# Kernel optimization log

Hardware: AMD Instinct MI355X
Metric: run time of the kernel (lower is better)

The kernel has to match this reference:

```python
import jax, jax.numpy as jnp
import numpy as np
from math import ceil, sqrt

# Inner module: Linear(2048,4096)+ReLU, Linear(4096,4096)+ReLU, Linear(4096,2048)
D_IN, D_H, D_OUT = 2048, 4096, 2048
BATCH = 4096
# named_modules() order: each Linear yields weight then bias; ReLU skipped
SHAPES = [(D_H, D_IN), (D_H,), (D_H, D_H), (D_H,), (D_OUT, D_H), (D_OUT,)]
NUM_P = sum(int(np.prod(s)) for s in SHAPES)  # 33_566_720
SIZE_N = ceil(sqrt(NUM_P))                    # 5794
SIZE_M = ceil(1.0 * SIZE_N / 2)               # 2897 (compress = 1.0)


def setup_inputs() -> dict:
    key = jax.random.key(0)
    k1, k2, k3 = jax.random.split(key, 3)
    k = sqrt(12) / 2 * SIZE_M ** (-0.25)  # norm_V init bound
    V1 = jax.random.uniform(k1, (SIZE_N, SIZE_M), jnp.float32, -k, k)
    V2 = jax.random.uniform(k2, (SIZE_M, SIZE_N), jnp.float32, -k, k)
    x = jax.random.normal(k3, (BATCH, D_IN), jnp.float32)
    return {"x": x, "V1": V1, "V2": V2}


def _unpack(Vf):
    # scatter-copy: contiguous slices of flattened V -> weights/biases in traversal order
    params, i = [], 0
    for s in SHAPES:
        n = int(np.prod(s))
        params.append(Vf[i:i + n].reshape(s))
        i += n
    return params


def reference(x, V1, V2):
    # WandBtoV: low-rank reconstruction then per-element copy into weights (fused here)
    Vf = (V1 @ V2).reshape(-1)  # [SIZE_N*SIZE_N]; only first NUM_P elements used
    W1, b1, W2, b2, W3, b3 = _unpack(Vf)
    h = jax.nn.relu(x @ W1.T + b1)   # [B, D_H]
    h = jax.nn.relu(h @ W2.T + b2)   # [B, D_H]
    return h @ W3.T + b3             # [B, D_OUT]
```

## Files before the change

### kernel.cpp

```cpp
#include <hip/hip_runtime.h>
#include <stdint.h>

typedef __attribute__((ext_vector_type(8)))  __bf16 bf16x8;
typedef __attribute__((ext_vector_type(16))) float  f32x16;
typedef unsigned short u16;
typedef __attribute__((ext_vector_type(8))) unsigned short u16x8;

#define GLOBAL_AS __attribute__((address_space(1)))
#define LDS_AS    __attribute__((address_space(3)))

__device__ __forceinline__ void load_lds16(const void* g, void* l) {
    __builtin_amdgcn_global_load_lds((const GLOBAL_AS void*)g, (LDS_AS void*)l, 16, 0, 0);
}

__device__ __forceinline__ u16 f2bf(float f) {
    union { float f; uint32_t u; } v; v.f = f;
    uint32_t r = v.u + 0x7FFFu + ((v.u >> 16) & 1u);
    return (u16)(r >> 16);
}
__device__ __forceinline__ float b2f(u16 b) {
    union { uint32_t u; float f; } v; v.u = ((uint32_t)b) << 16;
    return v.f;
}

__global__ void k_conv_pad(const float* __restrict__ in, u16* __restrict__ out,
                           int rIn, int cIn, int cOut, int total8) {
    int idx = blockIdx.x * blockDim.x + threadIdx.x;
    if (idx >= total8) return;
    int c8n = cOut >> 3;
    int r  = idx / c8n;
    int c0 = (idx - r * c8n) << 3;
    u16x8 o;
#pragma unroll
    for (int j = 0; j < 8; ++j) {
        int c = c0 + j;
        o[j] = (r < rIn && c < cIn) ? f2bf(in[(size_t)r * cIn + c]) : (u16)0;
    }
    *(u16x8*)(out + (size_t)r * cOut + c0) = o;
}

__global__ void k_transpose_conv(const float* __restrict__ in, u16* __restrict__ out,
                                 int kIn, int nIn, int kOut) {
    __shared__ float tile[32][33];
    int k0 = blockIdx.x * 32, n0 = blockIdx.y * 32;
    int tx = threadIdx.x, ty = threadIdx.y;
#pragma unroll
    for (int i = 0; i < 4; ++i) {
        int k = k0 + ty + i * 8, n = n0 + tx;
        tile[ty + i * 8][tx] = (k < kIn && n < nIn) ? in[(size_t)k * nIn + n] : 0.f;
    }
    __syncthreads();
#pragma unroll
    for (int i = 0; i < 4; ++i) {
        int n = n0 + ty + i * 8, k = k0 + tx;
        out[(size_t)n * kOut + k] = f2bf(tile[tx][ty + i * 8]);
    }
}

template <int MODE>
__global__ __launch_bounds__(256, 4) void k_gemm_bt(
    const u16* __restrict__ A, const u16* __restrict__ B,
    const u16* __restrict__ bias, void* __restrict__ Cv,
    int K, int ldc, int mReal, int nReal) {
    (void)bias;
    __shared__ __align__(16) char lds[32768];
    char* As = lds;
    char* Bs = lds + 16384;

    const int tid  = threadIdx.x;
    const int w    = tid >> 6, lane = tid & 63;
    const int l31  = lane & 31, hi = lane >> 5;
    const int wm   = (w & 1) * 64, wn = (w >> 1) * 64;
    const int bm   = blockIdx.y * 128, bn = blockIdx.x * 128;

    const int srcRow = tid >> 3;
    const int srcCol = (tid & 7) ^ (srcRow & 7);
    const u16* aSrc = A + (size_t)(bm + srcRow) * K + (srcCol << 3);
    const u16* bSrc = B + (size_t)(bn + srcRow) * K + (srcCol << 3);
    char* aDst = As + ((tid & ~63) << 4);
    char* bDst = Bs + ((tid & ~63) << 4);

    const int aRow0 = (wm + l31) * 128;
    const int aRow1 = (wm + 32 + l31) * 128;
    const int bRow0 = (wn + l31) * 128;
    const int bRow1 = (wn + 32 + l31) * 128;

    f32x16 acc[2][2];
#pragma unroll
    for (int i = 0; i < 2; ++i)
#pragma unroll
        for (int j = 0; j < 2; ++j) acc[i][j] = (f32x16)(0.f);

    for (int k0 = 0; k0 < K; k0 += 64) {
#pragma unroll
        for (int t = 0; t < 4; ++t) {
            load_lds16(aSrc + (size_t)(t * 32) * K, aDst + t * 4096);
            load_lds16(bSrc + (size_t)(t * 32) * K, bDst + t * 4096);
        }
        aSrc += 64; bSrc += 64;
        __syncthreads();
#pragma unroll
        for (int ks = 0; ks < 4; ++ks) {
            const int swz = (((ks * 2 + hi) ^ (l31 & 7)) << 4);
            bf16x8 af[2], bfr[2];
            af[0]  = *(const bf16x8*)(As + aRow0 + swz);
            af[1]  = *(const bf16x8*)(As + aRow1 + swz);
            bfr[0] = *(const bf16x8*)(Bs + bRow0 + swz);
            bfr[1] = *(const bf16x8*)(Bs + bRow1 + swz);
#pragma unroll
            for (int mi = 0; mi < 2; ++mi)
#pragma unroll
                for (int ni = 0; ni < 2; ++ni)
                    acc[mi][ni] = __builtin_amdgcn_mfma_f32_32x32x16_bf16(
                        af[mi], bfr[ni], acc[mi][ni], 0, 0, 0);
        }
        __syncthreads();
    }

    float bv[2];
    if (MODE >= 1) {
#pragma unroll
        for (int ni = 0; ni < 2; ++ni) bv[ni] = b2f(bias[bn + wn + ni * 32 + l31]);
    }
#pragma unroll
    for (int mi = 0; mi < 2; ++mi) {
#pragma unroll
        for (int reg = 0; reg < 16; ++reg) {
            int row = bm + wm + mi * 32 + (reg & 3) + 8 * (reg >> 2) + 4 * hi;
#pragma unroll
            for (int ni = 0; ni < 2; ++ni) {
                int col = bn + wn + ni * 32 + l31;
                float v = acc[mi][ni][reg];
                if (MODE == 0) {
                    if (row < mReal && col < nReal)
                        ((u16*)Cv)[(size_t)row * ldc + col] = f2bf(v);
                } else if (MODE == 1) {
                    v += bv[ni];
                    v = v > 0.f ? v : 0.f;
                    ((u16*)Cv)[(size_t)row * ldc + col] = f2bf(v);
                } else {
                    ((float*)Cv)[(size_t)row * ldc + col] = v + bv[ni];
                }
            }
        }
    }
}


#define BARRIER() do { asm volatile("" ::: "memory"); \
                       __builtin_amdgcn_s_barrier(); \
                       asm volatile("" ::: "memory"); } while (0)
#define LGKM0()   do { asm volatile("s_waitcnt lgkmcnt(0)" ::: "memory"); \
                       __builtin_amdgcn_sched_barrier(0); } while (0)
#define VMCNT0()  do { asm volatile("s_waitcnt vmcnt(0)" ::: "memory"); \
                       __builtin_amdgcn_sched_barrier(0); } while (0)

#define STAGE6(bb, koff) do { \
    _Pragma("unroll") for (int t = 0; t < 4; ++t) \
        load_lds16(aS + (koff) + (size_t)(t * 64) * K, (bb) + t * 4096 + wOff); \
    _Pragma("unroll") for (int t = 0; t < 2; ++t) \
        load_lds16(bS + (koff) + (size_t)(t * 64) * K, (bb) + 16384 + t * 4096 + wOff); \
} while (0)

#define RD6(bb, p, FA, FB) do { \
    const int co_ = ch0 ^ ((p) << 5); \
    FA[0] = *(const bf16x8*)((bb) + aR +    0 + co_); \
    FA[1] = *(const bf16x8*)((bb) + aR + 2048 + co_); \
    FA[2] = *(const bf16x8*)((bb) + aR + 4096 + co_); \
    FA[3] = *(const bf16x8*)((bb) + aR + 6144 + co_); \
    FB[0] = *(const bf16x8*)((bb) + bR +    0 + co_); \
    FB[1] = *(const bf16x8*)((bb) + bR + 2048 + co_); \
} while (0)

#define MM8(FA, FB) do { \
    __builtin_amdgcn_s_setprio(1); \
    acc[0][0] = __builtin_amdgcn_mfma_f32_32x32x16_bf16(FA[0], FB[0], acc[0][0], 0, 0, 0); \
    acc[1][0] = __builtin_amdgcn_mfma_f32_32x32x16_bf16(FA[1], FB[0], acc[1][0], 0, 0, 0); \
    acc[2][0] = __builtin_amdgcn_mfma_f32_32x32x16_bf16(FA[2], FB[0], acc[2][0], 0, 0, 0); \
    acc[3][0] = __builtin_amdgcn_mfma_f32_32x32x16_bf16(FA[3], FB[0], acc[3][0], 0, 0, 0); \
    acc[0][1] = __builtin_amdgcn_mfma_f32_32x32x16_bf16(FA[0], FB[1], acc[0][1], 0, 0, 0); \
    acc[1][1] = __builtin_amdgcn_mfma_f32_32x32x16_bf16(FA[1], FB[1], acc[1][1], 0, 0, 0); \
    acc[2][1] = __builtin_amdgcn_mfma_f32_32x32x16_bf16(FA[2], FB[1], acc[2][1], 0, 0, 0); \
    acc[3][1] = __builtin_amdgcn_mfma_f32_32x32x16_bf16(FA[3], FB[1], acc[3][1], 0, 0, 0); \
    __builtin_amdgcn_s_setprio(0); \
} while (0)

template <int MODE>
__global__ __launch_bounds__(256, 2) void k_gemm128(
    const u16* __restrict__ A, const u16* __restrict__ B,
    const u16* __restrict__ bias, void* __restrict__ Cv,
    int K, int ldc, int mReal, int nReal, int gx) {
    __shared__ __align__(16) char lds[49152];

    const int tid  = threadIdx.x;
    const int w    = tid >> 6, lane = tid & 63;
    const int l31  = lane & 31, hi = lane >> 5;
    const int wr   = w & 1, wc = w >> 1;

    const int nwg = (int)gridDim.x;
    const int q   = nwg >> 3, r = nwg & 7;
    const int xcd = (int)blockIdx.x & 7, lid = (int)blockIdx.x >> 3;
    const int wg  = (xcd < r ? xcd * (q + 1) : r * (q + 1) + (xcd - r) * q) + lid;
    const int bm  = (wg / gx) * 256;
    const int bn  = (wg % gx) * 128;

    char* const buf0 = lds;
    char* const buf1 = lds + 24576;

    const int srcRow = tid >> 2;
    const int srcCh  = (tid & 3) ^ ((srcRow >> 1) & 3);
    const int wOff   = (tid & ~63) << 4;

    const int aR  = (wr * 128 + l31) * 64;
    const int bR  = 16384 + (wc * 64 + l31) * 64;
    const int ch0 = ((hi ^ ((l31 >> 1) & 3))) << 4;

    const u16* const aS = A + (size_t)(bm + srcRow) * K + (srcCh << 3);
    const u16* const bS = B + (size_t)(bn + srcRow) * K + (srcCh << 3);

    f32x16 acc[4][2];
#pragma unroll
    for (int i = 0; i < 4; ++i)
#pragma unroll
        for (int j = 0; j < 2; ++j) acc[i][j] = (f32x16)(0.f);

    bf16x8 xa[4], xb[2], ya[4], yb[2];

    STAGE6(buf0, 0);
    VMCNT0();
    BARRIER();

    const int nIt = K >> 6;
    size_t ko = 0;
#pragma unroll 1
    for (int it = 0; it < nIt; ++it) {
        STAGE6(buf1, ko + 32);
        RD6(buf0, 0, xa, xb);
        RD6(buf0, 1, ya, yb);
        MM8(xa, xb);
        LGKM0(); VMCNT0(); BARRIER();
        if (it + 1 < nIt) { STAGE6(buf0, ko + 64); }
        MM8(ya, yb);
        RD6(buf1, 0, xa, xb);
        RD6(buf1, 1, ya, yb);
        MM8(xa, xb);
        LGKM0(); VMCNT0(); BARRIER();
        MM8(ya, yb);
        ko += 64;
    }

    float bv[2];
    if (MODE >= 1) {
#pragma unroll
        for (int ni = 0; ni < 2; ++ni) bv[ni] = b2f(bias[bn + wc * 64 + ni * 32 + l31]);
    }
#pragma unroll
    for (int mi = 0; mi < 4; ++mi) {
#pragma unroll
        for (int reg = 0; reg < 16; ++reg) {
            const int row = bm + wr * 128 + mi * 32 + (reg & 3) + 8 * (reg >> 2) + 4 * hi;
#pragma unroll
            for (int ni = 0; ni < 2; ++ni) {
                const int col = bn + wc * 64 + ni * 32 + l31;
                float vv = acc[mi][ni][reg];
                if (MODE == 0) {
                    if (row < mReal && col < nReal)
                        ((u16*)Cv)[(size_t)row * ldc + col] = f2bf(vv);
                } else if (MODE == 1) {
                    vv += bv[ni];
                    vv = vv > 0.f ? vv : 0.f;
                    ((u16*)Cv)[(size_t)row * ldc + col] = f2bf(vv);
                } else {
                    ((float*)Cv)[(size_t)row * ldc + col] = vv + bv[ni];
                }
            }
        }
    }
}

extern "C" void kernel_launch(void* const* d_in, const int* in_sizes, int n_in,
                              void* d_out, int out_size, void* d_ws, size_t ws_size,
                              hipStream_t stream) {
    (void)in_sizes; (void)n_in; (void)out_size; (void)ws_size;
    const float* x  = (const float*)d_in[0];
    const float* V1 = (const float*)d_in[1];
    const float* V2 = (const float*)d_in[2];

    char* ws = (char*)d_ws;
    u16* Vf   = (u16*)(ws);
    u16* V1b  = (u16*)(ws + 67141120);
    u16* V2bT = (u16*)(ws + 67141120 + 34668544);
    u16* Xb   = (u16*)(ws + 67141120 + 2 * 34668544);
    u16* H1   = V1b;
    u16* H2   = V2bT;

    k_conv_pad<<<8464, 256, 0, stream>>>(V1, V1b, 5794, 2897, 2944, 5888 * 2944 / 8);
    k_transpose_conv<<<dim3(92, 184), dim3(32, 8), 0, stream>>>(V2, V2bT, 2897, 5794, 2944);
    k_conv_pad<<<4096, 256, 0, stream>>>(x, Xb, 4096, 2048, 2048, 4096 * 2048 / 8);

    k_gemm128<0><<<1058, 256, 0, stream>>>(V1b, V2bT, nullptr, Vf,
                                           2944, 5794, 5794, 5794, 46);
    k_gemm128<1><<<512, 256, 0, stream>>>(Xb, Vf + 0, Vf + 8388608, H1,
                                          2048, 4096, 4096, 4096, 32);
    k_gemm128<1><<<512, 256, 0, stream>>>(H1, Vf + 8392704, Vf + 25169920, H2,
                                          4096, 4096, 4096, 4096, 32);
    k_gemm_bt<2><<<dim3(16, 32), 256, 0, stream>>>(H2, Vf + 25174016, Vf + 33562624, d_out,
                                                   4096, 2048, 4096, 2048);
}
```

Before: 752.6 us.

## Triple-buffer LDS pipeline in gemm128 and route final layer through it

Replaces the two-buffer, K=64-per-iteration loop with a three-buffer rotating pipeline over K=32 steps. It prefetches two stages ahead and waits only for the older stage (vmcnt 6), so global loads overlap more MFMA work. It also removes the simpler 128x128 k_gemm_bt kernel and runs the last layer through k_gemm128 MODE 2, which has a 256x128 tile and XCD-aware block remapping. LDS use grows to 72KB per block, which may reduce occupancy. The last layer now launches only 256 blocks, which could underfill the GPU.

```diff
diff --git a/kernel.cpp b/kernel.cpp
--- a/kernel.cpp
+++ b/kernel.cpp
@@ -57,109 +57,20 @@
     }
 }
 
-template <int MODE>
-__global__ __launch_bounds__(256, 4) void k_gemm_bt(
-    const u16* __restrict__ A, const u16* __restrict__ B,
-    const u16* __restrict__ bias, void* __restrict__ Cv,
-    int K, int ldc, int mReal, int nReal) {
-    (void)bias;
-    __shared__ __align__(16) char lds[32768];
-    char* As = lds;
-    char* Bs = lds + 16384;
-
-    const int tid  = threadIdx.x;
-    const int w    = tid >> 6, lane = tid & 63;
-    const int l31  = lane & 31, hi = lane >> 5;
-    const int wm   = (w & 1) * 64, wn = (w >> 1) * 64;
-    const int bm   = blockIdx.y * 128, bn = blockIdx.x * 128;
-
-    const int srcRow = tid >> 3;
-    const int srcCol = (tid & 7) ^ (srcRow & 7);
-    const u16* aSrc = A + (size_t)(bm + srcRow) * K + (srcCol << 3);
-    const u16* bSrc = B + (size_t)(bn + srcRow) * K + (srcCol << 3);
-    char* aDst = As + ((tid & ~63) << 4);
-    char* bDst = Bs + ((tid & ~63) << 4);
-
-    const int aRow0 = (wm + l31) * 128;
-    const int aRow1 = (wm + 32 + l31) * 128;
-    const int bRow0 = (wn + l31) * 128;
-    const int bRow1 = (wn + 32 + l31) * 128;
-
-    f32x16 acc[2][2];
-#pragma unroll
-    for (int i = 0; i < 2; ++i)
-#pragma unroll
-        for (int j = 0; j < 2; ++j) acc[i][j] = (f32x16)(0.f);
-
-    for (int k0 = 0; k0 < K; k0 += 64) {
-#pragma unroll
-        for (int t = 0; t < 4; ++t) {
-            load_lds16(aSrc + (size_t)(t * 32) * K, aDst + t * 4096);
-            load_lds16(bSrc + (size_t)(t * 32) * K, bDst + t * 4096);
-        }
-        aSrc += 64; bSrc += 64;
-        __syncthreads();
-#pragma unroll
-        for (int ks = 0; ks < 4; ++ks) {
-            const int swz = (((ks * 2 + hi) ^ (l31 & 7)) << 4);
-            bf16x8 af[2], bfr[2];
-            af[0]  = *(const bf16x8*)(As + aRow0 + swz);
-            af[1]  = *(const bf16x8*)(As + aRow1 + swz);
-            bfr[0] = *(const bf16x8*)(Bs + bRow0 + swz);
-            bfr[1] = *(const bf16x8*)(Bs + bRow1 + swz);
-#pragma unroll
-            for (int mi = 0; mi < 2; ++mi)
-#pragma unroll
-                for (int ni = 0; ni < 2; ++ni)
-                    acc[mi][ni] = __builtin_amdgcn_mfma_f32_32x32x16_bf16(
-                        af[mi], bfr[ni], acc[mi][ni], 0, 0, 0);
-        }
-        __syncthreads();
-    }
-
-    float bv[2];
-    if (MODE >= 1) {
-#pragma unroll
-        for (int ni = 0; ni < 2; ++ni) bv[ni] = b2f(bias[bn + wn + ni * 32 + l31]);
-    }
-#pragma unroll
-    for (int mi = 0; mi < 2; ++mi) {
-#pragma unroll
-        for (int reg = 0; reg < 16; ++reg) {
-            int row = bm + wm + mi * 32 + (reg & 3) + 8 * (reg >> 2) + 4 * hi;
-#pragma unroll
-            for (int ni = 0; ni < 2; ++ni) {
-                int col = bn + wn + ni * 32 + l31;
-                float v = acc[mi][ni][reg];
-                if (MODE == 0) {
-                    if (row < mReal && col < nReal)
-                        ((u16*)Cv)[(size_t)row * ldc + col] = f2bf(v);
-                } else if (MODE == 1) {
-                    v += bv[ni];
-                    v = v > 0.f ? v : 0.f;
-                    ((u16*)Cv)[(size_t)row * ldc + col] = f2bf(v);
-                } else {
-                    ((float*)Cv)[(size_t)row * ldc + col] = v + bv[ni];
-                }
-            }
-        }
-    }
-}
-
 
 #define BARRIER() do { asm volatile("" ::: "memory"); \
                        __builtin_amdgcn_s_barrier(); \
                        asm volatile("" ::: "memory"); } while (0)
 #define LGKM0()   do { asm volatile("s_waitcnt lgkmcnt(0)" ::: "memory"); \
                        __builtin_amdgcn_sched_barrier(0); } while (0)
-#define VMCNT0()  do { asm volatile("s_waitcnt vmcnt(0)" ::: "memory"); \
+#define VMCNT(n)  do { asm volatile("s_waitcnt vmcnt(" #n ")" ::: "memory"); \
                        __builtin_amdgcn_sched_barrier(0); } while (0)
 
 #define STAGE6(bb, koff) do { \
-    _Pragma("unroll") for (int t = 0; t < 4; ++t) \
-        load_lds16(aS + (koff) + (size_t)(t * 64) * K, (bb) + t * 4096 + wOff); \
-    _Pragma("unroll") for (int t = 0; t < 2; ++t) \
-        load_lds16(bS + (koff) + (size_t)(t * 64) * K, (bb) + 16384 + t * 4096 + wOff); \
+    _Pragma("unroll") for (int t_ = 0; t_ < 4; ++t_) \
+        load_lds16(aS + (koff) + (size_t)(t_ * 64) * K, (bb) + t_ * 4096 + wOff); \
+    _Pragma("unroll") for (int t_ = 0; t_ < 2; ++t_) \
+        load_lds16(bS + (koff) + (size_t)(t_ * 64) * K, (bb) + 16384 + t_ * 4096 + wOff); \
 } while (0)
 
 #define RD6(bb, p, FA, FB) do { \
@@ -190,7 +101,7 @@
     const u16* __restrict__ A, const u16* __restrict__ B,
     const u16* __restrict__ bias, void* __restrict__ Cv,
     int K, int ldc, int mReal, int nReal, int gx) {
-    __shared__ __align__(16) char lds[49152];
+    __shared__ __align__(16) char lds[73728];
 
     const int tid  = threadIdx.x;
     const int w    = tid >> 6, lane = tid & 63;
@@ -204,8 +115,9 @@
     const int bm  = (wg / gx) * 256;
     const int bn  = (wg % gx) * 128;
 
-    char* const buf0 = lds;
-    char* const buf1 = lds + 24576;
+    char* cb0 = lds;
+    char* cb1 = lds + 24576;
+    char* cb2 = lds + 49152;
 
     const int srcRow = tid >> 2;
     const int srcCh  = (tid & 3) ^ ((srcRow >> 1) & 3);
@@ -226,27 +138,27 @@
 
     bf16x8 xa[4], xb[2], ya[4], yb[2];
 
-    STAGE6(buf0, 0);
-    VMCNT0();
+    const int nT = K >> 5;
+
+    STAGE6(cb0, 0);
+    STAGE6(cb1, 32);
+    VMCNT(6);
     BARRIER();
 
-    const int nIt = K >> 6;
-    size_t ko = 0;
 #pragma unroll 1
-    for (int it = 0; it < nIt; ++it) {
-        STAGE6(buf1, ko + 32);
-        RD6(buf0, 0, xa, xb);
-        RD6(buf0, 1, ya, yb);
+    for (int t = 0; t < nT; ++t) {
+        if (t + 2 < nT) { STAGE6(cb2, (size_t)(t + 2) * 32); }
+        RD6(cb0, 0, xa, xb);
+        RD6(cb0, 1, ya, yb);
         MM8(xa, xb);
-        LGKM0(); VMCNT0(); BARRIER();
-        if (it + 1 < nIt) { STAGE6(buf0, ko + 64); }
         MM8(ya, yb);
-        RD6(buf1, 0, xa, xb);
-        RD6(buf1, 1, ya, yb);
-        MM8(xa, xb);
-        LGKM0(); VMCNT0(); BARRIER();
-        MM8(ya, yb);
-        ko += 64;
+        if (t + 1 < nT) {
+            LGKM0();
+            if (t + 2 < nT) { VMCNT(6); }
+            else           { VMCNT(0); }
+            BARRIER();
+        }
+        char* tp = cb0; cb0 = cb1; cb1 = cb2; cb2 = tp;
     }
 
     float bv[2];
@@ -304,6 +216,6 @@
                                           2048, 4096, 4096, 4096, 32);
     k_gemm128<1><<<512, 256, 0, stream>>>(H1, Vf + 8392704, Vf + 25169920, H2,
                                           4096, 4096, 4096, 4096, 32);
-    k_gemm_bt<2><<<dim3(16, 32), 256, 0, stream>>>(H2, Vf + 25174016, Vf + 33562624, d_out,
-                                                   4096, 2048, 4096, 2048);
-}
+    k_gemm128<2><<<256, 256, 0, stream>>>(H2, Vf + 25174016, Vf + 33562624, d_out,
+                                          4096, 2048, 4096, 2048, 16);
+}
```

Result: slower. 790.2 us (+5.0%).

## Switch main GEMM to 16x16x32 MFMA with new LDS swizzle and single-phase loop

Applied to the files above, without the earlier changes.

Replaces the 32x32x16 bf16 MFMA tiles with 16x16x32 MFMA in the 256x128 GEMM kernel, using an 8x4 grid of f32x4 accumulators per wave. The LDS staging layout, swizzle and fragment reads are rebuilt to match. The loop now reads each 32-wide K half-tile fully and runs one block of 32 MFMAs per half, instead of interleaving two half-phases. This aims to use a better-suited MFMA shape and simplify scheduling, but it drops the overlap between LDS reads and MFMAs within a phase and changes the output write pattern.

```diff
diff --git a/kernel.cpp b/kernel.cpp
--- a/kernel.cpp
+++ b/kernel.cpp
@@ -2,6 +2,7 @@
 #include <stdint.h>
 
 typedef __attribute__((ext_vector_type(8)))  __bf16 bf16x8;
+typedef __attribute__((ext_vector_type(4)))  float  f32x4;
 typedef __attribute__((ext_vector_type(16))) float  f32x16;
 typedef unsigned short u16;
 typedef __attribute__((ext_vector_type(8))) unsigned short u16x8;
@@ -156,37 +157,30 @@
                        __builtin_amdgcn_sched_barrier(0); } while (0)
 
 #define STAGE6(bb, koff) do { \
-    _Pragma("unroll") for (int t = 0; t < 4; ++t) \
-        load_lds16(aS + (koff) + (size_t)(t * 64) * K, (bb) + t * 4096 + wOff); \
-    _Pragma("unroll") for (int t = 0; t < 2; ++t) \
-        load_lds16(bS + (koff) + (size_t)(t * 64) * K, (bb) + 16384 + t * 4096 + wOff); \
+    _Pragma("unroll") for (int t_ = 0; t_ < 4; ++t_) \
+        load_lds16(aS + (koff) + (size_t)(t_ * 64) * K, (bb) + t_ * 4096 + ldsW); \
+    _Pragma("unroll") for (int t_ = 0; t_ < 2; ++t_) \
+        load_lds16(bS + (koff) + (size_t)(t_ * 64) * K, (bb) + 16384 + t_ * 4096 + ldsW); \
 } while (0)
 
-#define RD6(bb, p, FA, FB) do { \
-    const int co_ = ch0 ^ ((p) << 5); \
-    FA[0] = *(const bf16x8*)((bb) + aR +    0 + co_); \
-    FA[1] = *(const bf16x8*)((bb) + aR + 2048 + co_); \
-    FA[2] = *(const bf16x8*)((bb) + aR + 4096 + co_); \
-    FA[3] = *(const bf16x8*)((bb) + aR + 6144 + co_); \
-    FB[0] = *(const bf16x8*)((bb) + bR +    0 + co_); \
-    FB[1] = *(const bf16x8*)((bb) + bR + 2048 + co_); \
+#define RD12(bb) do { \
+    _Pragma("unroll") for (int mi = 0; mi < 8; ++mi) \
+        fa[mi] = *(const bf16x8*)((bb) + aRd + mi * 1024); \
+    _Pragma("unroll") for (int ni = 0; ni < 4; ++ni) \
+        fb[ni] = *(const bf16x8*)((bb) + bRd + ni * 1024); \
 } while (0)
 
-#define MM8(FA, FB) do { \
+#define MM32() do { \
     __builtin_amdgcn_s_setprio(1); \
-    acc[0][0] = __builtin_amdgcn_mfma_f32_32x32x16_bf16(FA[0], FB[0], acc[0][0], 0, 0, 0); \
-    acc[1][0] = __builtin_amdgcn_mfma_f32_32x32x16_bf16(FA[1], FB[0], acc[1][0], 0, 0, 0); \
-    acc[2][0] = __builtin_amdgcn_mfma_f32_32x32x16_bf16(FA[2], FB[0], acc[2][0], 0, 0, 0); \
-    acc[3][0] = __builtin_amdgcn_mfma_f32_32x32x16_bf16(FA[3], FB[0], acc[3][0], 0, 0, 0); \
-    acc[0][1] = __builtin_amdgcn_mfma_f32_32x32x16_bf16(FA[0], FB[1], acc[0][1], 0, 0, 0); \
-    acc[1][1] = __builtin_amdgcn_mfma_f32_32x32x16_bf16(FA[1], FB[1], acc[1][1], 0, 0, 0); \
-    acc[2][1] = __builtin_amdgcn_mfma_f32_32x32x16_bf16(FA[2], FB[1], acc[2][1], 0, 0, 0); \
-    acc[3][1] = __builtin_amdgcn_mfma_f32_32x32x16_bf16(FA[3], FB[1], acc[3][1], 0, 0, 0); \
+    _Pragma("unroll") for (int ni = 0; ni < 4; ++ni) \
+    _Pragma("unroll") for (int mi = 0; mi < 8; ++mi) \
+        acc[mi][ni] = __builtin_amdgcn_mfma_f32_16x16x32_bf16( \
+            fa[mi], fb[ni], acc[mi][ni], 0, 0, 0); \
     __builtin_amdgcn_s_setprio(0); \
 } while (0)
 
 template <int MODE>
-__global__ __launch_bounds__(256, 2) void k_gemm128(
+__global__ __launch_bounds__(256, 2) void k_gemm2b(
     const u16* __restrict__ A, const u16* __restrict__ B,
     const u16* __restrict__ bias, void* __restrict__ Cv,
     int K, int ldc, int mReal, int nReal, int gx) {
@@ -194,7 +188,7 @@
 
     const int tid  = threadIdx.x;
     const int w    = tid >> 6, lane = tid & 63;
-    const int l31  = lane & 31, hi = lane >> 5;
+    const int l15  = lane & 15, lg4 = lane >> 4;
     const int wr   = w & 1, wc = w >> 1;
 
     const int nwg = (int)gridDim.x;
@@ -207,24 +201,24 @@
     char* const buf0 = lds;
     char* const buf1 = lds + 24576;
 
-    const int srcRow = tid >> 2;
-    const int srcCh  = (tid & 3) ^ ((srcRow >> 1) & 3);
-    const int wOff   = (tid & ~63) << 4;
-
-    const int aR  = (wr * 128 + l31) * 64;
-    const int bR  = 16384 + (wc * 64 + l31) * 64;
-    const int ch0 = ((hi ^ ((l31 >> 1) & 3))) << 4;
-
-    const u16* const aS = A + (size_t)(bm + srcRow) * K + (srcCh << 3);
-    const u16* const bS = B + (size_t)(bn + srcRow) * K + (srcCh << 3);
-
-    f32x16 acc[4][2];
-#pragma unroll
-    for (int i = 0; i < 4; ++i)
-#pragma unroll
-        for (int j = 0; j < 2; ++j) acc[i][j] = (f32x16)(0.f);
-
-    bf16x8 xa[4], xb[2], ya[4], yb[2];
+    const int cOrig = (lane & 3) ^ ((lane >> 2) & 3);
+    const int sRow  = w * 16 + (lane >> 2);
+    const int ldsW  = w * 1024;
+
+    const int slotOff = ((lg4 ^ (l15 & 3)) << 4);
+    const int aRd = (wr * 128 + l15) * 64 + slotOff;
+    const int bRd = 16384 + (wc * 64 + l15) * 64 + slotOff;
+
+    const u16* const aS = A + (size_t)(bm + sRow) * K + cOrig * 8;
+    const u16* const bS = B + (size_t)(bn + sRow) * K + cOrig * 8;
+
+    f32x4 acc[8][4];
+#pragma unroll
+    for (int i = 0; i < 8; ++i)
+#pragma unroll
+        for (int j = 0; j < 4; ++j) acc[i][j] = (f32x4)(0.f);
+
+    bf16x8 fa[8], fb[4];
 
     STAGE6(buf0, 0);
     VMCNT0();
@@ -235,34 +229,32 @@
 #pragma unroll 1
     for (int it = 0; it < nIt; ++it) {
         STAGE6(buf1, ko + 32);
-        RD6(buf0, 0, xa, xb);
-        RD6(buf0, 1, ya, yb);
-        MM8(xa, xb);
-        LGKM0(); VMCNT0(); BARRIER();
+        RD12(buf0);
+        LGKM0();
+        MM32();
+        VMCNT0(); BARRIER();
         if (it + 1 < nIt) { STAGE6(buf0, ko + 64); }
-        MM8(ya, yb);
-        RD6(buf1, 0, xa, xb);
-        RD6(buf1, 1, ya, yb);
-        MM8(xa, xb);
-        LGKM0(); VMCNT0(); BARRIER();
-        MM8(ya, yb);
+        RD12(buf1);
+        LGKM0();
+        MM32();
+        VMCNT0(); BARRIER();
         ko += 64;
     }
 
-    float bv[2];
+    float bv[4];
     if (MODE >= 1) {
 #pragma unroll
-        for (int ni = 0; ni < 2; ++ni) bv[ni] = b2f(bias[bn + wc * 64 + ni * 32 + l31]);
-    }
-#pragma unroll
-    for (int mi = 0; mi < 4; ++mi) {
-#pragma unroll
-        for (int reg = 0; reg < 16; ++reg) {
-            const int row = bm + wr * 128 + mi * 32 + (reg & 3) + 8 * (reg >> 2) + 4 * hi;
-#pragma unroll
-            for (int ni = 0; ni < 2; ++ni) {
-                const int col = bn + wc * 64 + ni * 32 + l31;
-                float vv = acc[mi][ni][reg];
+        for (int ni = 0; ni < 4; ++ni) bv[ni] = b2f(bias[bn + wc * 64 + ni * 16 + l15]);
+    }
+#pragma unroll
+    for (int mi = 0; mi < 8; ++mi) {
+#pragma unroll
+        for (int ni = 0; ni < 4; ++ni) {
+#pragma unroll
+            for (int rg = 0; rg < 4; ++rg) {
+                const int row = bm + wr * 128 + mi * 16 + lg4 * 4 + rg;
+                const int col = bn + wc * 64 + ni * 16 + l15;
+                float vv = acc[mi][ni][rg];
                 if (MODE == 0) {
                     if (row < mReal && col < nReal)
                         ((u16*)Cv)[(size_t)row * ldc + col] = f2bf(vv);
@@ -298,12 +290,12 @@
     k_transpose_conv<<<dim3(92, 184), dim3(32, 8), 0, stream>>>(V2, V2bT, 2897, 5794, 2944);
     k_conv_pad<<<4096, 256, 0, stream>>>(x, Xb, 4096, 2048, 2048, 4096 * 2048 / 8);
 
-    k_gemm128<0><<<1058, 256, 0, stream>>>(V1b, V2bT, nullptr, Vf,
-                                           2944, 5794, 5794, 5794, 46);
-    k_gemm128<1><<<512, 256, 0, stream>>>(Xb, Vf + 0, Vf + 8388608, H1,
-                                          2048, 4096, 4096, 4096, 32);
-    k_gemm128<1><<<512, 256, 0, stream>>>(H1, Vf + 8392704, Vf + 25169920, H2,
-                                          4096, 4096, 4096, 4096, 32);
+    k_gemm2b<0><<<1058, 256, 0, stream>>>(V1b, V2bT, nullptr, Vf,
+                                          2944, 5794, 5794, 5794, 46);
+    k_gemm2b<1><<<512, 256, 0, stream>>>(Xb, Vf + 0, Vf + 8388608, H1,
+                                         2048, 4096, 4096, 4096, 32);
+    k_gemm2b<1><<<512, 256, 0, stream>>>(H1, Vf + 8392704, Vf + 25169920, H2,
+                                         4096, 4096, 4096, 4096, 32);
     k_gemm_bt<2><<<dim3(16, 32), 256, 0, stream>>>(H2, Vf + 25174016, Vf + 33562624, d_out,
                                                    4096, 2048, 4096, 2048);
 }
```

After: 728.5 us. 1.03x faster.
